# Optimization experiments

Measured on AMD Instinct MI355X. Metric: run time of the kernel, lower is better.

Reference implementation:

```python
import jax, jax.numpy as jnp
import numpy as np

B, N, E = 2, 2048, 2048
H, D = 16, 128
BASE = 10000.0


def rope(t, offset=0):
    # t: [b, n, h, d] -- rotary position embedding (Lrpe type 1), half-rotation form
    d = t.shape[-1]
    pos = jnp.arange(t.shape[1], dtype=jnp.float32) + offset
    inv = BASE ** (-jnp.arange(0, d, 2, dtype=jnp.float32) / d)  # [d/2]
    ang = pos[:, None] * inv[None, :]                            # [n, d/2]
    cos = jnp.cos(ang)[None, :, None, :]
    sin = jnp.sin(ang)[None, :, None, :]
    t1, t2 = t[..., : d // 2], t[..., d // 2 :]
    return jnp.concatenate([t1 * cos - t2 * sin, t2 * cos + t1 * sin], axis=-1)


def setup_inputs() -> dict:
    key = jax.random.key(0)
    ks = jax.random.split(key, 6)
    s = lambda k, shape, fan: jax.random.normal(k, shape, jnp.float32) / np.sqrt(fan)
    return {
        "x": jax.random.normal(ks[0], (B, N, E), jnp.float32),
        "Wq": s(ks[1], (H * D, E), E),      # q_proj.weight
        "Wkv": s(ks[2], (2 * D, E), E),     # kv_proj.weight
        "Wkvh": s(ks[3], (2 * H, E), E),    # kv_head_proj.weight
        "Wg": s(ks[4], (2 * H, E), E),      # gate_proj.weight (gate_type=1)
        "Wout": s(ks[5], (E, H * D), H * D) # out_proj.weight
    }


def reference(x, Wq, Wkv, Wkvh, Wg, Wout):
    b, n, _ = x.shape
    q = (x @ Wq.T).reshape(b, n, H, D)
    kv = x @ Wkv.T            # [b, n, 2D]
    kv_head = x @ Wkvh.T      # [b, n, 2H] (mpa_type=0, activation 'none')

    # gate_type == 1: log-sigmoid gated cumulative-sum decay on kv_head (GLA-style)
    g = x @ Wg.T                                                       # [b, n, 2H]
    log_f = jnp.concatenate(
        [jnp.zeros((b, 1, 2 * H), jnp.float32), jax.nn.log_sigmoid(g)], axis=1
    )
    log_f_cumsum = jnp.cumsum(log_f, axis=1)[:, :-1]                   # [b, n, 2H]
    kv_head = kv_head * jnp.exp(log_f_cumsum)
    kv_head = jnp.cumsum(kv_head, axis=1)

    kp, vp = kv[..., :D], kv[..., D:]
    kh, vh = kv_head[..., :H], kv_head[..., H:]
    # low-rank KV expansion: outer product of shared (d) with per-head scalar (h)
    k = jnp.einsum('bnd,bnh->bnhd', kp, kh)
    v = jnp.einsum('bnd,bnh->bnhd', vp, vh)

    q = rope(q)
    k = rope(k)

    # causal softmax attention (flash_attn_func equivalent), scale = D**-0.5
    scale = 1.0 / np.sqrt(D)
    scores = jnp.einsum('bnhd,bmhd->bhnm', q, k) * scale
    mask = jnp.tril(jnp.ones((n, n), bool))
    scores = jnp.where(mask[None, None], scores, -jnp.inf)
    p = jax.nn.softmax(scores, axis=-1)
    o = jnp.einsum('bhnm,bmhd->bnhd', p, v).reshape(b, n, H * D)
    return o @ Wout.T
```

## Files before the change

### kernel.cpp

```cpp
#include <hip/hip_runtime.h>
#include <hip/hip_bf16.h>
#include <math.h>

typedef __attribute__((ext_vector_type(8))) short bf16x8;
typedef __attribute__((ext_vector_type(4))) float f32x4;

#define MFMA16(a, b, c) __builtin_amdgcn_mfma_f32_16x16x32_bf16((a), (b), (c), 0, 0, 0)

static __device__ __forceinline__ float fast_exp2(float x) { return __builtin_amdgcn_exp2f(x); }

static __device__ __forceinline__ unsigned short f2bf(float f) {
  __hip_bfloat16 h = __float2bfloat16(f);
  unsigned short u;
  __builtin_memcpy(&u, &h, 2);
  return u;
}
static __device__ __forceinline__ float bf2f(unsigned short u) {
  unsigned int x = ((unsigned int)u) << 16;
  float f;
  __builtin_memcpy(&f, &x, 4);
  return f;
}

static __device__ __forceinline__ void cast8(const float* __restrict__ src,
                                             unsigned short* __restrict__ dst, int blk, int tid) {
  int i = (blk * 256 + tid) * 8;
  float4 a = *(const float4*)(src + i);
  float4 b = *(const float4*)(src + i + 4);
  union { unsigned short u[8]; bf16x8 v; } o;
  o.u[0] = f2bf(a.x); o.u[1] = f2bf(a.y); o.u[2] = f2bf(a.z); o.u[3] = f2bf(a.w);
  o.u[4] = f2bf(b.x); o.u[5] = f2bf(b.y); o.u[6] = f2bf(b.z); o.u[7] = f2bf(b.w);
  *(bf16x8*)(dst + i) = o.v;
}

__global__ __launch_bounds__(256) void prep(const float* __restrict__ x, const float* __restrict__ Wq,
                                            const float* __restrict__ Wout, const float* __restrict__ Wkv,
                                            const float* __restrict__ Wkvh, const float* __restrict__ Wg,
                                            unsigned short* __restrict__ x_bf, unsigned short* __restrict__ wq_bf,
                                            unsigned short* __restrict__ wout_bf, unsigned short* __restrict__ wsm_bf,
                                            float2* __restrict__ cs, float* __restrict__ wgt) {
  int bid = blockIdx.x, tid = threadIdx.x;
  if (bid < 4096) {
    cast8(x, x_bf, bid, tid);
  } else if (bid < 6144) {
    cast8(Wq, wq_bf, bid - 4096, tid);
  } else if (bid < 8192) {
    cast8(Wout, wout_bf, bid - 6144, tid);
  } else if (bid < 8576) {
    int row = bid - 8192;
    int c = tid * 8;
    const float* src = nullptr;
    if (row < 256) src = Wkv + (size_t)row * 2048;
    else if (row < 288) src = Wkvh + (size_t)(row - 256) * 2048;
    union { unsigned short u[8]; bf16x8 v; } o;
    if (src) {
      float4 a = *(const float4*)(src + c);
      float4 b = *(const float4*)(src + c + 4);
      o.u[0] = f2bf(a.x); o.u[1] = f2bf(a.y); o.u[2] = f2bf(a.z); o.u[3] = f2bf(a.w);
      o.u[4] = f2bf(b.x); o.u[5] = f2bf(b.y); o.u[6] = f2bf(b.z); o.u[7] = f2bf(b.w);
    } else {
      for (int j = 0; j < 8; j++) o.u[j] = 0;
    }
    *(bf16x8*)(wsm_bf + (size_t)row * 2048 + c) = o.v;
  } else if (bid < 9088) {
    int i = (bid - 8576) * 256 + tid;
    int f = i & 63, n = i >> 6;
    float inv = powf(10000.0f, -(float)(2 * f) / 128.0f);
    float ang = (float)n * inv;
    cs[i] = make_float2(cosf(ang), sinf(ang));
  } else {
    int i = (bid - 9088) * 256 + tid;
    int oc = i >> 11, k = i & 2047;
    wgt[(size_t)k * 32 + oc] = Wg[i];
  }
}

__global__ __launch_bounds__(256) void gproj(const float* __restrict__ x, const float* __restrict__ Wgt,
                                             float* __restrict__ lsg_t) {
  int tid = blockIdx.x * 256 + threadIdx.x;
  int tok = tid >> 5, oc = tid & 31;
  const float* xr = x + (size_t)tok * 2048;
  float acc = 0.f;
  for (int k = 0; k < 2048; k += 4) {
    float4 a = *(const float4*)(xr + k);
    acc += a.x * Wgt[(size_t)k * 32 + oc] + a.y * Wgt[(size_t)(k + 1) * 32 + oc] +
           a.z * Wgt[(size_t)(k + 2) * 32 + oc] + a.w * Wgt[(size_t)(k + 3) * 32 + oc];
  }
  float ls = (acc >= 0.f) ? -log1pf(expf(-acc)) : acc - log1pf(expf(acc));
  int b = tok >> 11, n = tok & 2047;
  lsg_t[((size_t)(b * 32 + oc)) * 2048 + n] = ls;
}

__global__ __launch_bounds__(256) void scan_kernel(const float* __restrict__ lsg_t,
                                                   const float* __restrict__ so,
                                                   float* __restrict__ khvh) {
  int b = blockIdx.x >> 5, ch = blockIdx.x & 31;
  int t = threadIdx.x, lane = t & 63, wv = t >> 6;
  const float* L = lsg_t + ((size_t)(b * 32 + ch)) * 2048 + t * 8;
  float ls[8], v[8];
  float4 a = *(const float4*)L, c = *(const float4*)(L + 4);
  ls[0] = a.x; ls[1] = a.y; ls[2] = a.z; ls[3] = a.w;
  ls[4] = c.x; ls[5] = c.y; ls[6] = c.z; ls[7] = c.w;
  const float* V = so + ((size_t)(b * 2048 + t * 8)) * 384 + 256 + ch;
#pragma unroll
  for (int j = 0; j < 8; j++) v[j] = V[(size_t)j * 384];
  float run = 0.f;
#pragma unroll
  for (int j = 0; j < 8; j++) run += ls[j];
  float incl = run;
#pragma unroll
  for (int off = 1; off < 64; off <<= 1) {
    float nv = __shfl_up(incl, off);
    if (lane >= off) incl += nv;
  }
  __shared__ float ws[2][4];
  if (lane == 63) ws[0][wv] = incl;
  __syncthreads();
  float wbase = 0.f;
#pragma unroll
  for (int w = 0; w < 4; w++) wbase += (w < wv) ? ws[0][w] : 0.f;
  float baseA = wbase + incl - run;
  float lf = baseA, s = 0.f;
#pragma unroll
  for (int j = 0; j < 8; j++) { s += v[j] * __expf(lf); lf += ls[j]; }
  float incl2 = s;
#pragma unroll
  for (int off = 1; off < 64; off <<= 1) {
    float nv = __shfl_up(incl2, off);
    if (lane >= off) incl2 += nv;
  }
  if (lane == 63) ws[1][wv] = incl2;
  __syncthreads();
  float wbase2 = 0.f;
#pragma unroll
  for (int w = 0; w < 4; w++) wbase2 += (w < wv) ? ws[1][w] : 0.f;
  float base2 = wbase2 + incl2 - s;
  lf = baseA; s = base2;
  float* O = khvh + ((size_t)(b * 2048 + t * 8)) * 32 + ch;
#pragma unroll
  for (int j = 0; j < 8; j++) { s += v[j] * __expf(lf); lf += ls[j]; O[(size_t)j * 32] = s; }
}

__global__ __launch_bounds__(256) void build_kv(const float* __restrict__ small_out,
                                                const float* __restrict__ khvh,
                                                const float2* __restrict__ cs,
                                                unsigned short* __restrict__ k_r,
                                                unsigned short* __restrict__ v_r) {
  int tok = blockIdx.x;
  int b = tok >> 11, n = tok & 2047;
  __shared__ float kpr[128], vps[128], khs[16], vhs[16];
  int t = threadIdx.x;
  const float* so = small_out + (size_t)tok * 384;
  if (t < 64) {
    float k1 = so[t], k2 = so[t + 64];
    float2 c = cs[(n << 6) + t];
    kpr[t] = k1 * c.x - k2 * c.y;
    kpr[t + 64] = k2 * c.x + k1 * c.y;
  } else if (t < 192) {
    int d = t - 64;
    vps[d] = so[128 + d];
  } else if (t < 224) {
    int ch = t - 192;
    float v = khvh[(size_t)tok * 32 + ch];
    if (ch < 16) khs[ch] = v; else vhs[ch - 16] = v;
  }
  __syncthreads();
  int h = t >> 4, d0 = (t & 15) * 8;
  float kh = khs[h], vh = vhs[h];
  union { unsigned short u[8]; bf16x8 v; } ko, vo;
#pragma unroll
  for (int j = 0; j < 8; j++) {
    ko.u[j] = f2bf(kpr[d0 + j] * kh);
    vo.u[j] = f2bf(vps[d0 + j] * vh);
  }
  size_t off = (((size_t)b * 16 + h) * 2048 + n) * 128 + d0;
  *(bf16x8*)(k_r + off) = ko.v;
  *(bf16x8*)(v_r + off) = vo.v;
}

__global__ __launch_bounds__(256) void transpose_v(const unsigned short* __restrict__ v_r,
                                                   unsigned short* __restrict__ v_t) {
  int nt = blockIdx.x;
  int bh = blockIdx.y;
  __shared__ unsigned short Ts[64 * 136];
  int tid = threadIdx.x;
  const unsigned short* src = v_r + ((size_t)bh * 2048 + nt * 64) * 128;
#pragma unroll
  for (int c = 0; c < 4; c++) {
    int g = c * 256 + tid;
    int r = g >> 4, ch = (g & 15) * 8;
    *(bf16x8*)&Ts[r * 136 + ch] = *(const bf16x8*)(src + r * 128 + ch);
  }
  __syncthreads();
#pragma unroll
  for (int c = 0; c < 4; c++) {
    int g = c * 256 + tid;
    int d = g >> 3, nc = (g & 7) * 8;
    union { unsigned short u[8]; bf16x8 v; } o;
#pragma unroll
    for (int j = 0; j < 8; j++) o.u[j] = Ts[(nc + j) * 136 + d];
    *(bf16x8*)(v_t + ((size_t)bh * 128 + d) * 2048 + nt * 64 + nc) = o.v;
  }
}

template <int MODE>
__global__ __launch_bounds__(256) void gemm_bt(const unsigned short* __restrict__ A,
                                               const unsigned short* __restrict__ B,
                                               float* __restrict__ Cf,
                                               unsigned short* __restrict__ Cb,
                                               int K, int ldc) {
  __shared__ unsigned short As[128 * 32];
  __shared__ unsigned short Bs[128 * 32];
  int tid = threadIdx.x;
  int wave = tid >> 6, lane = tid & 63, l15 = lane & 15, lg = lane >> 4;
  int wr = wave >> 1, wc = wave & 1;
  int lin = blockIdx.y * gridDim.x + blockIdx.x;
  int cpx = (gridDim.x * gridDim.y) >> 3;
  int swz = (lin & 7) * cpx + (lin >> 3);
  int bx = swz % gridDim.x, by = swz / gridDim.x;
  int row0 = by * 128, col0 = bx * 128;
  f32x4 acc[4][4];
#pragma unroll
  for (int m = 0; m < 4; m++)
#pragma unroll
    for (int n = 0; n < 4; n++) acc[m][n] = (f32x4){0.f, 0.f, 0.f, 0.f};

  for (int k0 = 0; k0 < K; k0 += 32) {
#pragma unroll
    for (int c = 0; c < 2; c++) {
      int chunk = c * 256 + tid;
      int r = chunk >> 2, kk = (chunk & 3) * 8;
      __builtin_amdgcn_global_load_lds(
          (const __attribute__((address_space(1))) void*)(A + (size_t)(row0 + r) * K + k0 + kk),
          (__attribute__((address_space(3))) void*)(As + ((size_t)c * 256 + wave * 64) * 8), 16, 0, 0);
      __builtin_amdgcn_global_load_lds(
          (const __attribute__((address_space(1))) void*)(B + (size_t)(col0 + r) * K + k0 + kk),
          (__attribute__((address_space(3))) void*)(Bs + ((size_t)c * 256 + wave * 64) * 8), 16, 0, 0);
    }
    __syncthreads();
    bf16x8 af[4], bfr[4];
#pragma unroll
    for (int m = 0; m < 4; m++) af[m] = *(const bf16x8*)&As[(wr * 64 + m * 16 + l15) * 32 + lg * 8];
#pragma unroll
    for (int n = 0; n < 4; n++) bfr[n] = *(const bf16x8*)&Bs[(wc * 64 + n * 16 + l15) * 32 + lg * 8];
#pragma unroll
    for (int m = 0; m < 4; m++)
#pragma unroll
      for (int n = 0; n < 4; n++) acc[m][n] = MFMA16(af[m], bfr[n], acc[m][n]);
    __syncthreads();
  }
#pragma unroll
  for (int m = 0; m < 4; m++) {
    int row_b = row0 + wr * 64 + m * 16 + lg * 4;
#pragma unroll
    for (int n = 0; n < 4; n++) {
      int col = col0 + wc * 64 + n * 16 + l15;
#pragma unroll
      for (int j = 0; j < 4; j++) {
        int row = row_b + j;
        if (MODE == 0) {
          Cf[(size_t)row * ldc + col] = acc[m][n][j];
        } else {
          int b = row >> 11, nn = row & 2047, h = col >> 7, d = col & 127;
          Cb[(((size_t)b * 16 + h) * 2048 + nn) * 128 + d] = f2bf(acc[m][n][j]);
        }
      }
    }
  }
}

__global__ __launch_bounds__(256, 2) void flash_attn(const unsigned short* __restrict__ q_r,
                                                     const unsigned short* __restrict__ k_r,
                                                     const unsigned short* __restrict__ v_t,
                                                     const float2* __restrict__ cs,
                                                     unsigned short* __restrict__ o) {
  int lin = blockIdx.y * 16 + blockIdx.x;
  int swz = (lin & 7) * 64 + (lin >> 3);
  int bx = swz & 15, bh = swz >> 4;
  const unsigned short* Kg = k_r + (size_t)bh * 2048 * 128;
  const unsigned short* Vtg = v_t + (size_t)bh * 128 * 2048;
  __shared__ unsigned short Ks[2][64 * 128];
  __shared__ unsigned short VTs[2][128 * 64];
  __shared__ unsigned short Ps[4][16 * 72];
  int tid = threadIdx.x, wave = tid >> 6, lane = tid & 63, l15 = lane & 15, lg = lane >> 4;
  int sw = (l15 & 7) * 8;
  int b = bh >> 4, h = bh & 15;

  union { unsigned short u[8]; bf16x8 v; } onesu;
#pragma unroll
  for (int j = 0; j < 8; j++) onesu.u[j] = 0x3F80;
  const bf16x8 ones = onesu.v;

  int qtA = bx, qtB = 31 - bx;
  int qt = qtA;

  bf16x8 qf[4];
#define LOAD_Q()                                                                                   \
  {                                                                                                \
    const unsigned short* Qg = q_r + ((size_t)bh * 2048 + qt * 64) * 128;                          \
    int n = qt * 64 + wave * 16 + l15;                                                             \
    union { unsigned short u[8]; bf16x8 v; } r0, r1, r2, r3;                                       \
    r0.v = *(const bf16x8*)(Qg + (wave * 16 + l15) * 128 + 0 * 32 + lg * 8);                       \
    r1.v = *(const bf16x8*)(Qg + (wave * 16 + l15) * 128 + 1 * 32 + lg * 8);                       \
    r2.v = *(const bf16x8*)(Qg + (wave * 16 + l15) * 128 + 2 * 32 + lg * 8);                       \
    r3.v = *(const bf16x8*)(Qg + (wave * 16 + l15) * 128 + 3 * 32 + lg * 8);                       \
    union { unsigned short u[8]; bf16x8 v; } o0, o1, o2, o3;                                       \
    _Pragma("unroll") for (int j = 0; j < 8; j++) {                                                \
      float2 c0 = cs[(n << 6) + 0 * 32 + lg * 8 + j];                                              \
      float t1 = bf2f(r0.u[j]), t2 = bf2f(r2.u[j]);                                                \
      o0.u[j] = f2bf(t1 * c0.x - t2 * c0.y);                                                       \
      o2.u[j] = f2bf(t2 * c0.x + t1 * c0.y);                                                       \
      float2 c1 = cs[(n << 6) + 1 * 32 + lg * 8 + j];                                              \
      float s1 = bf2f(r1.u[j]), s2 = bf2f(r3.u[j]);                                                \
      o1.u[j] = f2bf(s1 * c1.x - s2 * c1.y);                                                       \
      o3.u[j] = f2bf(s2 * c1.x + s1 * c1.y);                                                       \
    }                                                                                              \
    qf[0] = o0.v; qf[1] = o1.v; qf[2] = o2.v; qf[3] = o3.v;                                        \
  }

  LOAD_Q();

  float m_r[4], l_r[4];
  f32x4 oacc[8];
#pragma unroll
  for (int j = 0; j < 4; j++) { m_r[j] = -INFINITY; l_r[j] = 0.f; }
#pragma unroll
  for (int db = 0; db < 8; db++) oacc[db] = (f32x4){0.f, 0.f, 0.f, 0.f};

  const float kscale = 0.12753102f;
  const float THR = 11.0f;

#define STAGE(kt, bsel)                                                                           \
  {                                                                                               \
    int kti = (kt);                                                                               \
    int bs = (bsel);                                                                              \
    _Pragma("unroll") for (int c = 0; c < 4; c++) {                                               \
      int s = c * 256 + tid;                                                                      \
      int kr = s >> 4, kc = ((s & 15) ^ (kr & 7)) * 8;                                            \
      __builtin_amdgcn_global_load_lds(                                                           \
          (const __attribute__((address_space(1))) void*)(Kg + (size_t)(kti * 64 + kr) * 128 + kc),\
          (__attribute__((address_space(3))) void*)(&Ks[bs][(c * 256 + wave * 64) * 8]), 16, 0, 0);\
      int vr = s >> 3, vc = ((s & 7) ^ (vr & 7)) * 8;                                             \
      __builtin_amdgcn_global_load_lds(                                                           \
          (const __attribute__((address_space(1))) void*)(Vtg + (size_t)vr * 2048 + kti * 64 + vc),\
          (__attribute__((address_space(3))) void*)(&VTs[bs][(c * 256 + wave * 64) * 8]), 16, 0, 0);\
    }                                                                                             \
  }

  STAGE(0, 0);
  __syncthreads();

  for (int s = 0; s < 33; ++s) {
    int nb = s & 1;
    if (s + 1 < 33) {
      int nk = (s + 1 <= qtA) ? (s + 1) : (s + 1 - (qtA + 1));
      STAGE(nk, nb ^ 1);
    }
    int kt = (s <= qtA) ? s : (s - (qtA + 1));
    bool diag = (s == qtA) || (s == 32);
    int qrow0 = qt * 64 + wave * 16 + lg * 4;

    f32x4 sc[4];
#pragma unroll
    for (int cb = 0; cb < 4; cb++) sc[cb] = (f32x4){0.f, 0.f, 0.f, 0.f};
    __builtin_amdgcn_s_setprio(1);
#pragma unroll
    for (int kk = 0; kk < 4; kk++) {
#pragma unroll
      for (int cb = 0; cb < 4; cb++) {
        bf16x8 kf = *(const bf16x8*)&Ks[nb][(cb * 16 + l15) * 128 + ((kk * 32 + lg * 8) ^ sw)];
        sc[cb] = MFMA16(qf[kk], kf, sc[cb]);
      }
    }
    __builtin_amdgcn_s_setprio(0);
    if (diag) {
#pragma unroll
      for (int cb = 0; cb < 4; cb++) {
        int col = kt * 64 + cb * 16 + l15;
#pragma unroll
        for (int j = 0; j < 4; j++) {
          float v = sc[cb][j] * kscale;
          if (col > qrow0 + j) v = -INFINITY;
          sc[cb][j] = v;
        }
      }
    } else {
#pragma unroll
      for (int cb = 0; cb < 4; cb++)
#pragma unroll
        for (int j = 0; j < 4; j++) sc[cb][j] *= kscale;
    }
    float pm[4];
#pragma unroll
    for (int j = 0; j < 4; j++)
      pm[j] = fmaxf(fmaxf(sc[0][j], sc[1][j]), fmaxf(sc[2][j], sc[3][j]));
    bool grow = !__all((pm[0] <= m_r[0] + THR) & (pm[1] <= m_r[1] + THR) &
                       (pm[2] <= m_r[2] + THR) & (pm[3] <= m_r[3] + THR));
    if (grow) {
#pragma unroll
      for (int off = 1; off < 16; off <<= 1) {
#pragma unroll
        for (int j = 0; j < 4; j++) pm[j] = fmaxf(pm[j], __shfl_xor(pm[j], off));
      }
#pragma unroll
      for (int j = 0; j < 4; j++) {
        float mn = fmaxf(m_r[j], pm[j]);
        float corr = fast_exp2(m_r[j] - mn);
        m_r[j] = mn;
        l_r[j] *= corr;
#pragma unroll
        for (int db = 0; db < 8; db++) oacc[db][j] *= corr;
      }
    }
#pragma unroll
    for (int cb = 0; cb < 4; cb++)
#pragma unroll
      for (int j = 0; j < 4; j++)
        Ps[wave][(lg * 4 + j) * 72 + cb * 16 + l15] = f2bf(fast_exp2(sc[cb][j] - m_r[j]));
    f32x4 sacc = (f32x4){0.f, 0.f, 0.f, 0.f};
    __builtin_amdgcn_s_setprio(1);
#pragma unroll
    for (int kc = 0; kc < 2; kc++) {
      bf16x8 pa = *(const bf16x8*)&Ps[wave][l15 * 72 + kc * 32 + lg * 8];
      sacc = MFMA16(pa, ones, sacc);
#pragma unroll
      for (int db = 0; db < 8; db++) {
        bf16x8 vb = *(const bf16x8*)&VTs[nb][(db * 16 + l15) * 64 + ((kc * 32 + lg * 8) ^ sw)];
        oacc[db] = MFMA16(pa, vb, oacc[db]);
      }
    }
    __builtin_amdgcn_s_setprio(0);
#pragma unroll
    for (int j = 0; j < 4; j++) l_r[j] += sacc[j];
    __syncthreads();

    if (s == qtA) {
      int qrow_e = qt * 64 + wave * 16 + lg * 4;
#pragma unroll
      for (int db = 0; db < 8; db++) {
        int d = db * 16 + l15;
#pragma unroll
        for (int j = 0; j < 4; j++) {
          float val = oacc[db][j] / l_r[j];
          o[((size_t)(b * 2048 + qrow_e + j)) * 2048 + h * 128 + d] = f2bf(val);
        }
      }
      qt = qtB;
      LOAD_Q();
#pragma unroll
      for (int j = 0; j < 4; j++) { m_r[j] = -INFINITY; l_r[j] = 0.f; }
#pragma unroll
      for (int db = 0; db < 8; db++) oacc[db] = (f32x4){0.f, 0.f, 0.f, 0.f};
    }
  }
  int qrow_e = qt * 64 + wave * 16 + lg * 4;
#pragma unroll
  for (int db = 0; db < 8; db++) {
    int d = db * 16 + l15;
#pragma unroll
    for (int j = 0; j < 4; j++) {
      float val = oacc[db][j] / l_r[j];
      o[((size_t)(b * 2048 + qrow_e + j)) * 2048 + h * 128 + d] = f2bf(val);
    }
  }
#undef STAGE
#undef LOAD_Q
}

extern "C" void kernel_launch(void* const* d_in, const int* in_sizes, int n_in,
                              void* d_out, int out_size, void* d_ws, size_t ws_size,
                              hipStream_t stream) {
  (void)in_sizes; (void)n_in; (void)out_size; (void)ws_size;
  const float* x    = (const float*)d_in[0];
  const float* Wq   = (const float*)d_in[1];
  const float* Wkv  = (const float*)d_in[2];
  const float* Wkvh = (const float*)d_in[3];
  const float* Wg   = (const float*)d_in[4];
  const float* Wout = (const float*)d_in[5];
  float* out = (float*)d_out;

  char* ws = (char*)d_ws;
  size_t off = 0;
  auto alloc = [&](size_t bytes) -> void* {
    void* p = ws + off;
    off += (bytes + 255) & ~(size_t)255;
    return p;
  };
  unsigned short* x_bf    = (unsigned short*)alloc(4096ull * 2048 * 2);
  unsigned short* wq_bf   = (unsigned short*)alloc(2048ull * 2048 * 2);
  unsigned short* wout_bf = (unsigned short*)alloc(2048ull * 2048 * 2);
  unsigned short* wsm_bf  = (unsigned short*)alloc(384ull * 2048 * 2);
  unsigned short* q_r     = (unsigned short*)alloc(4096ull * 2048 * 2);
  unsigned short* k_r     = (unsigned short*)alloc(4096ull * 2048 * 2);
  unsigned short* v_r     = (unsigned short*)alloc(4096ull * 2048 * 2);
  unsigned short* o_bf    = (unsigned short*)alloc(4096ull * 2048 * 2);
  float* small_out        = (float*)alloc(4096ull * 384 * 4);
  float* lsg_t            = (float*)alloc(64ull * 2048 * 4);
  float* khvh             = (float*)alloc(4096ull * 32 * 4);
  float2* cs              = (float2*)alloc(2048ull * 64 * 8);
  float* wgt              = (float*)alloc(2048ull * 32 * 4);
  unsigned short* v_t     = x_bf;

  prep<<<9344, 256, 0, stream>>>(x, Wq, Wout, Wkv, Wkvh, Wg, x_bf, wq_bf, wout_bf, wsm_bf, cs, wgt);
  gproj<<<512, 256, 0, stream>>>(x, wgt, lsg_t);
  gemm_bt<0><<<dim3(3, 32), 256, 0, stream>>>(x_bf, wsm_bf, small_out, nullptr, 2048, 384);
  gemm_bt<2><<<dim3(16, 32), 256, 0, stream>>>(x_bf, wq_bf, nullptr, q_r, 2048, 2048);
  scan_kernel<<<64, 256, 0, stream>>>(lsg_t, small_out, khvh);
  build_kv<<<4096, 256, 0, stream>>>(small_out, khvh, cs, k_r, v_r);
  transpose_v<<<dim3(32, 32), 256, 0, stream>>>(v_r, v_t);
  flash_attn<<<dim3(16, 32), 256, 0, stream>>>(q_r, k_r, v_t, cs, o_bf);
  gemm_bt<0><<<dim3(16, 32), 256, 0, stream>>>(o_bf, wout_bf, out, nullptr, 2048, 2048);
}
```

Before: 320.3 us.

## Pipeline GEMM loads with 4-stage LDS ring and fuse KV build with V transpose

The GEMM main loop now uses a four-buffer LDS ring, prefetching three K-tiles ahead. It relies on explicit vmcnt waits and a single barrier per iteration, which hides global-to-LDS latency behind the MFMA work, and it raises MFMA priority with setprio. Separately, build_kv and transpose_v are merged into one kernel that writes V directly in transposed layout, removing the v_r intermediate buffer and one kernel launch. The ring quadruples LDS use per GEMM block, which may reduce occupancy, and the hand-counted vmcnt values must match the number of loads issued per stage.

```diff
diff --git a/kernel.cpp b/kernel.cpp
--- a/kernel.cpp
+++ b/kernel.cpp
@@ -141,65 +141,65 @@
   for (int j = 0; j < 8; j++) { s += v[j] * __expf(lf); lf += ls[j]; O[(size_t)j * 32] = s; }
 }
 
-__global__ __launch_bounds__(256) void build_kv(const float* __restrict__ small_out,
-                                                const float* __restrict__ khvh,
-                                                const float2* __restrict__ cs,
-                                                unsigned short* __restrict__ k_r,
-                                                unsigned short* __restrict__ v_r) {
-  int tok = blockIdx.x;
-  int b = tok >> 11, n = tok & 2047;
-  __shared__ float kpr[128], vps[128], khs[16], vhs[16];
+__global__ __launch_bounds__(256) void build_kv2(const float* __restrict__ so,
+                                                 const float* __restrict__ khvh,
+                                                 const float2* __restrict__ cs,
+                                                 unsigned short* __restrict__ k_r,
+                                                 unsigned short* __restrict__ v_t) {
+  int ntb = blockIdx.x, bh = blockIdx.y;
+  int b = bh >> 4, h = bh & 15;
+  int tok0 = b * 2048 + ntb * 64;
+  int n0 = ntb * 64;
+  __shared__ float khs[64], vhs[64];
+  __shared__ unsigned short Vt_s[64 * 132];
   int t = threadIdx.x;
-  const float* so = small_out + (size_t)tok * 384;
   if (t < 64) {
-    float k1 = so[t], k2 = so[t + 64];
-    float2 c = cs[(n << 6) + t];
-    kpr[t] = k1 * c.x - k2 * c.y;
-    kpr[t + 64] = k2 * c.x + k1 * c.y;
-  } else if (t < 192) {
-    int d = t - 64;
-    vps[d] = so[128 + d];
-  } else if (t < 224) {
-    int ch = t - 192;
-    float v = khvh[(size_t)tok * 32 + ch];
-    if (ch < 16) khs[ch] = v; else vhs[ch - 16] = v;
+    khs[t] = khvh[(size_t)(tok0 + t) * 32 + h];
+    vhs[t] = khvh[(size_t)(tok0 + t) * 32 + 16 + h];
   }
   __syncthreads();
-  int h = t >> 4, d0 = (t & 15) * 8;
-  float kh = khs[h], vh = vhs[h];
-  union { unsigned short u[8]; bf16x8 v; } ko, vo;
-#pragma unroll
-  for (int j = 0; j < 8; j++) {
-    ko.u[j] = f2bf(kpr[d0 + j] * kh);
-    vo.u[j] = f2bf(vps[d0 + j] * vh);
-  }
-  size_t off = (((size_t)b * 16 + h) * 2048 + n) * 128 + d0;
-  *(bf16x8*)(k_r + off) = ko.v;
-  *(bf16x8*)(v_r + off) = vo.v;
-}
-
-__global__ __launch_bounds__(256) void transpose_v(const unsigned short* __restrict__ v_r,
-                                                   unsigned short* __restrict__ v_t) {
-  int nt = blockIdx.x;
-  int bh = blockIdx.y;
-  __shared__ unsigned short Ts[64 * 136];
-  int tid = threadIdx.x;
-  const unsigned short* src = v_r + ((size_t)bh * 2048 + nt * 64) * 128;
 #pragma unroll
   for (int c = 0; c < 4; c++) {
-    int g = c * 256 + tid;
-    int r = g >> 4, ch = (g & 15) * 8;
-    *(bf16x8*)&Ts[r * 136 + ch] = *(const bf16x8*)(src + r * 128 + ch);
+    int idx = c * 256 + t;
+    int r = idx >> 4, q4 = (idx & 15) * 4;
+    const float* sop = so + (size_t)(tok0 + r) * 384;
+    float4 k1 = *(const float4*)(sop + q4);
+    float4 k2 = *(const float4*)(sop + 64 + q4);
+    float kh = khs[r];
+    int n = n0 + r;
+    union { unsigned short u[4]; uint2 v2; } o1, o2;
+#pragma unroll
+    for (int j = 0; j < 4; j++) {
+      float2 cc = cs[(n << 6) + q4 + j];
+      float av = ((const float*)&k1)[j], bv = ((const float*)&k2)[j];
+      o1.u[j] = f2bf((av * cc.x - bv * cc.y) * kh);
+      o2.u[j] = f2bf((bv * cc.x + av * cc.y) * kh);
+    }
+    size_t off = ((size_t)bh * 2048 + n) * 128 + q4;
+    *(uint2*)(k_r + off) = o1.v2;
+    *(uint2*)(k_r + off + 64) = o2.v2;
+  }
+#pragma unroll
+  for (int c = 0; c < 8; c++) {
+    int idx = c * 256 + t;
+    int r = idx >> 5, d4 = (idx & 31) * 4;
+    const float* sop = so + (size_t)(tok0 + r) * 384 + 128;
+    float4 v = *(const float4*)(sop + d4);
+    float vh = vhs[r];
+    union { unsigned short u[4]; uint2 v2; } ov;
+#pragma unroll
+    for (int j = 0; j < 4; j++) ov.u[j] = f2bf(((const float*)&v)[j] * vh);
+    *(uint2*)&Vt_s[r * 132 + d4] = ov.v2;
   }
   __syncthreads();
 #pragma unroll
   for (int c = 0; c < 4; c++) {
-    int g = c * 256 + tid;
-    int d = g >> 3, nc = (g & 7) * 8;
+    int idx = c * 256 + t;
+    int d = idx >> 3, c8 = (idx & 7) * 8;
     union { unsigned short u[8]; bf16x8 v; } o;
 #pragma unroll
-    for (int j = 0; j < 8; j++) o.u[j] = Ts[(nc + j) * 136 + d];
-    *(bf16x8*)(v_t + ((size_t)bh * 128 + d) * 2048 + nt * 64 + nc) = o.v;
+    for (int j = 0; j < 8; j++) o.u[j] = Vt_s[(c8 + j) * 132 + d];
+    *(bf16x8*)(v_t + ((size_t)bh * 128 + d) * 2048 + n0 + c8) = o.v;
   }
 }
 
@@ -209,8 +209,8 @@
                                                float* __restrict__ Cf,
                                                unsigned short* __restrict__ Cb,
                                                int K, int ldc) {
-  __shared__ unsigned short As[128 * 32];
-  __shared__ unsigned short Bs[128 * 32];
+  __shared__ unsigned short As[4][128 * 32];
+  __shared__ unsigned short Bs[4][128 * 32];
   int tid = threadIdx.x;
   int wave = tid >> 6, lane = tid & 63, l15 = lane & 15, lg = lane >> 4;
   int wr = wave >> 1, wc = wave & 1;
@@ -225,30 +225,55 @@
 #pragma unroll
     for (int n = 0; n < 4; n++) acc[m][n] = (f32x4){0.f, 0.f, 0.f, 0.f};
 
-  for (int k0 = 0; k0 < K; k0 += 32) {
-#pragma unroll
-    for (int c = 0; c < 2; c++) {
-      int chunk = c * 256 + tid;
-      int r = chunk >> 2, kk = (chunk & 3) * 8;
-      __builtin_amdgcn_global_load_lds(
-          (const __attribute__((address_space(1))) void*)(A + (size_t)(row0 + r) * K + k0 + kk),
-          (__attribute__((address_space(3))) void*)(As + ((size_t)c * 256 + wave * 64) * 8), 16, 0, 0);
-      __builtin_amdgcn_global_load_lds(
-          (const __attribute__((address_space(1))) void*)(B + (size_t)(col0 + r) * K + k0 + kk),
-          (__attribute__((address_space(3))) void*)(Bs + ((size_t)c * 256 + wave * 64) * 8), 16, 0, 0);
-    }
-    __syncthreads();
+#define STAGE_T(kti, bs)                                                                           \
+  {                                                                                                \
+    int k0_ = (kti) * 32;                                                                          \
+    _Pragma("unroll") for (int c = 0; c < 2; c++) {                                                \
+      int chunk = c * 256 + tid;                                                                   \
+      int r = chunk >> 2, kk = (chunk & 3) * 8;                                                    \
+      __builtin_amdgcn_global_load_lds(                                                            \
+          (const __attribute__((address_space(1))) void*)(A + (size_t)(row0 + r) * K + k0_ + kk),  \
+          (__attribute__((address_space(3))) void*)(&As[bs][((size_t)c * 256 + wave * 64) * 8]),   \
+          16, 0, 0);                                                                               \
+      __builtin_amdgcn_global_load_lds(                                                            \
+          (const __attribute__((address_space(1))) void*)(B + (size_t)(col0 + r) * K + k0_ + kk),  \
+          (__attribute__((address_space(3))) void*)(&Bs[bs][((size_t)c * 256 + wave * 64) * 8]),   \
+          16, 0, 0);                                                                               \
+    }                                                                                              \
+  }
+
+  int nt = K >> 5;
+  STAGE_T(0, 0);
+  STAGE_T(1, 1);
+  STAGE_T(2, 2);
+
+  for (int t = 0; t < nt; ++t) {
+    int cur = t & 3;
+    int ahead = nt - 1 - t;
+    if (ahead > 2) ahead = 2;
+    if (ahead == 2) asm volatile("s_waitcnt vmcnt(8)" ::: "memory");
+    else if (ahead == 1) asm volatile("s_waitcnt vmcnt(4)" ::: "memory");
+    else asm volatile("s_waitcnt vmcnt(0)" ::: "memory");
+    __builtin_amdgcn_sched_barrier(0);
+    __builtin_amdgcn_s_barrier();
+    __builtin_amdgcn_sched_barrier(0);
+    if (t + 3 < nt) STAGE_T(t + 3, (t + 3) & 3);
     bf16x8 af[4], bfr[4];
 #pragma unroll
-    for (int m = 0; m < 4; m++) af[m] = *(const bf16x8*)&As[(wr * 64 + m * 16 + l15) * 32 + lg * 8];
-#pragma unroll
-    for (int n = 0; n < 4; n++) bfr[n] = *(const bf16x8*)&Bs[(wc * 64 + n * 16 + l15) * 32 + lg * 8];
-#pragma unroll
     for (int m = 0; m < 4; m++)
+      af[m] = *(const bf16x8*)&As[cur][(wr * 64 + m * 16 + l15) * 32 + lg * 8];
+#pragma unroll
+    for (int n = 0; n < 4; n++)
+      bfr[n] = *(const bf16x8*)&Bs[cur][(wc * 64 + n * 16 + l15) * 32 + lg * 8];
+    __builtin_amdgcn_s_setprio(1);
+#pragma unroll
+    for (int m = 0; m < 4; m++)
 #pragma unroll
       for (int n = 0; n < 4; n++) acc[m][n] = MFMA16(af[m], bfr[n], acc[m][n]);
-    __syncthreads();
-  }
+    __builtin_amdgcn_s_setprio(0);
+  }
+#undef STAGE_T
+
 #pragma unroll
   for (int m = 0; m < 4; m++) {
     int row_b = row0 + wr * 64 + m * 16 + lg * 4;
@@ -492,7 +517,6 @@
   unsigned short* wsm_bf  = (unsigned short*)alloc(384ull * 2048 * 2);
   unsigned short* q_r     = (unsigned short*)alloc(4096ull * 2048 * 2);
   unsigned short* k_r     = (unsigned short*)alloc(4096ull * 2048 * 2);
-  unsigned short* v_r     = (unsigned short*)alloc(4096ull * 2048 * 2);
   unsigned short* o_bf    = (unsigned short*)alloc(4096ull * 2048 * 2);
   float* small_out        = (float*)alloc(4096ull * 384 * 4);
   float* lsg_t            = (float*)alloc(64ull * 2048 * 4);
@@ -506,8 +530,7 @@
   gemm_bt<0><<<dim3(3, 32), 256, 0, stream>>>(x_bf, wsm_bf, small_out, nullptr, 2048, 384);
   gemm_bt<2><<<dim3(16, 32), 256, 0, stream>>>(x_bf, wq_bf, nullptr, q_r, 2048, 2048);
   scan_kernel<<<64, 256, 0, stream>>>(lsg_t, small_out, khvh);
-  build_kv<<<4096, 256, 0, stream>>>(small_out, khvh, cs, k_r, v_r);
-  transpose_v<<<dim3(32, 32), 256, 0, stream>>>(v_r, v_t);
+  build_kv2<<<dim3(32, 32), 256, 0, stream>>>(small_out, khvh, cs, k_r, v_t);
   flash_attn<<<dim3(16, 32), 256, 0, stream>>>(q_r, k_r, v_t, cs, o_bf);
   gemm_bt<0><<<dim3(16, 32), 256, 0, stream>>>(o_bf, wout_bf, out, nullptr, 2048, 2048);
 }
```

New measurement: 303.4 us. 5.3% less time.
